# Kernel optimization log

Measured on AMD Instinct MI355X. Metric: run time of the kernel, lower is better.

The kernel has to match this reference:

```python
import jax, jax.numpy as jnp
import numpy as np

D_MODEL = 1024
NUM_HEADS = 16
NUM_KV_HEADS = 4
D_K = D_MODEL // NUM_HEADS  # 64
GROUP = NUM_HEADS // NUM_KV_HEADS  # 4
ROPE_BASE = 10000.0
NEG = -10000.0


def _rope_cos_sin(seq_len, d_k, dtype):
    # matches standard RotaryEmbedding: inv_freq over even dims, emb = cat(freqs, freqs)
    inv_freq = 1.0 / (ROPE_BASE ** (jnp.arange(0, d_k, 2, dtype=jnp.float32) / d_k))
    t = jnp.arange(seq_len, dtype=jnp.float32)
    freqs = jnp.einsum('s,f->sf', t, inv_freq)          # [S, d_k/2]
    emb = jnp.concatenate([freqs, freqs], axis=-1)       # [S, d_k]
    return jnp.cos(emb).astype(dtype), jnp.sin(emb).astype(dtype)


def _apply_rope(x, cos, sin):
    # x: [B, H, S, d_k]; cos/sin: [S, d_k] broadcast over B, H
    half = x.shape[-1] // 2
    x1, x2 = x[..., :half], x[..., half:]
    rotated = jnp.concatenate([-x2, x1], axis=-1)
    return x * cos + rotated * sin


def setup_inputs() -> dict:
    key = jax.random.key(0)
    ks = jax.random.split(key, 7)
    B, S = 2, 2048
    scale = 1.0 / np.sqrt(D_MODEL)
    return {
        'query': jax.random.normal(ks[0], (B, S, D_MODEL), dtype=jnp.float32),
        'key': jax.random.normal(ks[1], (B, S, D_MODEL), dtype=jnp.float32),
        'value': jax.random.normal(ks[2], (B, S, D_MODEL), dtype=jnp.float32),
        'Wq': jax.random.normal(ks[3], (D_MODEL, D_MODEL), dtype=jnp.float32) * scale,
        'Wk': jax.random.normal(ks[4], (NUM_KV_HEADS * D_K, D_MODEL), dtype=jnp.float32) * scale,
        'Wv': jax.random.normal(ks[5], (NUM_KV_HEADS * D_K, D_MODEL), dtype=jnp.float32) * scale,
        'Wo': jax.random.normal(ks[6], (D_MODEL, D_MODEL), dtype=jnp.float32) * scale,
    }


def reference(query, key, value, Wq, Wk, Wv, Wo):
    B, Sq, _ = query.shape
    Sk = key.shape[1]
    # projections (nn.Linear: x @ W.T)
    Q = (query @ Wq.T).reshape(B, Sq, NUM_HEADS, D_K).transpose(0, 2, 1, 3)      # [B,H,Sq,dk]
    K = (key @ Wk.T).reshape(B, Sk, NUM_KV_HEADS, D_K).transpose(0, 2, 1, 3)      # [B,Hkv,Sk,dk]
    V = (value @ Wv.T).reshape(B, Sk, NUM_KV_HEADS, D_K).transpose(0, 2, 1, 3)    # [B,Hkv,Sk,dk]
    # RoPE
    cos, sin = _rope_cos_sin(Sq, D_K, Q.dtype)
    Q = _apply_rope(Q, cos, sin)
    K = _apply_rope(K, cos[:Sk], sin[:Sk])
    # GQA attention without explicitly materializing expanded K/V:
    # group query heads as [B, Hkv, G, Sq, dk]
    Qg = Q.reshape(B, NUM_KV_HEADS, GROUP, Sq, D_K)
    scores = jnp.einsum('bhgqd,bhkd->bhgqk', Qg, K) / jnp.sqrt(jnp.float32(D_K))  # [B,Hkv,G,Sq,Sk]
    causal = jnp.tril(jnp.ones((Sq, Sk), dtype=bool))
    scores = jnp.where(causal, scores, jnp.float32(NEG))
    probs = jax.nn.softmax(scores, axis=-1)
    out = jnp.einsum('bhgqk,bhkd->bhgqd', probs, V)                                # [B,Hkv,G,Sq,dk]
    out = out.reshape(B, NUM_HEADS, Sq, D_K).transpose(0, 2, 1, 3).reshape(B, Sq, D_MODEL)
    return out @ Wo.T
```

## Files before the change

### kernel.cpp

```cpp
#include <hip/hip_runtime.h>
#include <hip/hip_bf16.h>
#include <stdint.h>

typedef __attribute__((ext_vector_type(4))) float f32x4;
typedef __attribute__((ext_vector_type(8))) short short8;

#define S_LEN 2048
#define BATCH 2
#define NH 16
#define NKV 4
#define DK 64
#define LOG2E 1.44269504f

__device__ __forceinline__ ushort f2bf(float f) {
  union { float f; uint32_t u; } v; v.f = f;
  uint32_t u = v.u;
  u += 0x7fff + ((u >> 16) & 1);
  return (ushort)(u >> 16);
}
__device__ __forceinline__ float bf2f(ushort h) {
  union { uint32_t u; float f; } v; v.u = ((uint32_t)h) << 16;
  return v.f;
}

__device__ __forceinline__ void gld16(const ushort* g, ushort* l) {
  __builtin_amdgcn_global_load_lds((const __attribute__((address_space(1))) void*)g,
                                   (__attribute__((address_space(3))) void*)l,
                                   16, 0, 0);
}

template<int CTRL>
__device__ __forceinline__ float dpp_movf(float x) {
  return __int_as_float(__builtin_amdgcn_update_dpp(0, __float_as_int(x), CTRL, 0xF, 0xF, true));
}
__device__ __forceinline__ float rowred_sum16(float v) {
  v += dpp_movf<0xB1>(v);
  v += dpp_movf<0x4E>(v);
  v += dpp_movf<0x141>(v);
  v += dpp_movf<0x140>(v);
  return v;
}

__global__ void cvt3_kernel(const float* __restrict__ q, const float* __restrict__ k,
                            const float* __restrict__ v, ushort* __restrict__ oq,
                            ushort* __restrict__ ok, ushort* __restrict__ ov) {
  int i = blockIdx.x * blockDim.x + threadIdx.x;
  if (i >= 1048576) return;
  const float* in = blockIdx.y == 0 ? q : (blockIdx.y == 1 ? k : v);
  ushort* out = blockIdx.y == 0 ? oq : (blockIdx.y == 1 ? ok : ov);
  float4 x = ((const float4*)in)[i];
  ushort4 o;
  o.x = f2bf(x.x); o.y = f2bf(x.y); o.z = f2bf(x.z); o.w = f2bf(x.w);
  ((ushort4*)out)[i] = o;
}

__global__ void cvtW_kernel(const float* __restrict__ w0, const float* __restrict__ w1,
                            const float* __restrict__ w2, const float* __restrict__ w3,
                            ushort* __restrict__ o0, ushort* __restrict__ o1,
                            ushort* __restrict__ o2, ushort* __restrict__ o3) {
  int y = blockIdx.y;
  int n4 = (y == 0 || y == 3) ? 262144 : 65536;
  int i = blockIdx.x * blockDim.x + threadIdx.x;
  if (i >= n4) return;
  const float* in = y == 0 ? w0 : y == 1 ? w1 : y == 2 ? w2 : w3;
  ushort* out = y == 0 ? o0 : y == 1 ? o1 : y == 2 ? o2 : o3;
  float4 x = ((const float4*)in)[i];
  ushort4 o;
  o.x = f2bf(x.x); o.y = f2bf(x.y); o.z = f2bf(x.z); o.w = f2bf(x.w);
  ((ushort4*)out)[i] = o;
}

__global__ void rope_table_kernel(float* __restrict__ tab) {
  int i = blockIdx.x * blockDim.x + threadIdx.x;
  int s = i >> 5, f = i & 31;
  float freq = (float)s * powf(10000.0f, -(float)f / 32.0f);
  tab[i] = cosf(freq);
  tab[65536 + i] = sinf(freq);
}

template<int EPI>
__device__ __forceinline__ void gemm_body(const ushort* __restrict__ A,
                                          const ushort* __restrict__ W,
                                          void* __restrict__ Cout,
                                          const float* __restrict__ tab,
                                          int N, int K, int bx, int by,
                                          ushort* Al, ushort* Wl) {
  const int t = threadIdx.x;
  const int lane = t & 63;
  const int w = t >> 6;
  const int wr = w >> 1, wc = w & 1;
  const int m0 = bx * 128, n0 = by * 128;
  const int g = lane >> 4, q16 = lane & 15;

  f32x4 acc[4][4] = {};

  const int lrow = lane >> 2, lcol = (lane & 3) * 8;
  const ushort* Ap = A + (size_t)(m0 + w * 32 + lrow) * K + lcol;
  const ushort* Wp = W + (size_t)(n0 + w * 32 + lrow) * K + lcol;
  ushort* Ab0 = &Al[(w * 32) * 32];
  ushort* Ab1 = &Al[(w * 32 + 16) * 32];
  ushort* Wb0 = &Wl[(w * 32) * 32];
  ushort* Wb1 = &Wl[(w * 32 + 16) * 32];

  const int KSTEPS = K >> 5;
  for (int kt = 0; kt < KSTEPS; ++kt) {
    const int k0 = kt << 5;
    __syncthreads();
    gld16(Ap + k0, Ab0);
    gld16(Ap + (size_t)16 * K + k0, Ab1);
    gld16(Wp + k0, Wb0);
    gld16(Wp + (size_t)16 * K + k0, Wb1);
    __syncthreads();
    short8 af[4], wf[4];
    #pragma unroll
    for (int i = 0; i < 4; ++i)
      af[i] = *(const short8*)&Al[(wr * 64 + i * 16 + q16) * 32 + g * 8];
    #pragma unroll
    for (int j = 0; j < 4; ++j)
      wf[j] = *(const short8*)&Wl[(wc * 64 + j * 16 + q16) * 32 + g * 8];
    #pragma unroll
    for (int i = 0; i < 4; ++i)
      #pragma unroll
      for (int j = 0; j < 4; ++j)
        acc[i][j] = __builtin_amdgcn_mfma_f32_16x16x32_bf16(af[i], wf[j], acc[i][j], 0, 0, 0);
  }

  if (EPI == 0) {
    #pragma unroll
    for (int i = 0; i < 4; ++i)
      #pragma unroll
      for (int j = 0; j < 4; ++j) {
        int row0 = m0 + wr * 64 + i * 16 + g * 4;
        int col  = n0 + wc * 64 + j * 16 + q16;
        #pragma unroll
        for (int r = 0; r < 4; ++r)
          ((float*)Cout)[(size_t)(row0 + r) * N + col] = acc[i][j][r];
      }
  } else if (EPI == 1 || EPI == 2) {
    const int NHE = (EPI == 1) ? NH : NKV;
    const float qscale = (EPI == 1) ? 0.125f * LOG2E : 1.0f;
    const int h = (n0 + wc * 64) >> 6;
    ushort* O = (ushort*)Cout;
    #pragma unroll
    for (int i = 0; i < 4; ++i)
      #pragma unroll
      for (int j = 0; j < 2; ++j) {
        const int d = j * 16 + q16;
        #pragma unroll
        for (int r = 0; r < 4; ++r) {
          int row = m0 + wr * 64 + i * 16 + g * 4 + r;
          int b = row >> 11, s = row & 2047;
          float x1 = acc[i][j][r], x2 = acc[i][j + 2][r];
          float c = tab[s * 32 + d], sn = tab[65536 + s * 32 + d];
          ushort* base = O + ((size_t)(b * NHE + h) * 2048 + s) * 64;
          base[d]      = f2bf((x1 * c - x2 * sn) * qscale);
          base[d + 32] = f2bf((x2 * c + x1 * sn) * qscale);
        }
      }
  } else {
    const int h = (n0 + wc * 64) >> 6;
    ushort* O = (ushort*)Cout;
    #pragma unroll
    for (int i = 0; i < 4; ++i) {
      int row0 = m0 + wr * 64 + i * 16 + g * 4;
      int b = row0 >> 11, s0 = row0 & 2047;
      #pragma unroll
      for (int j = 0; j < 4; ++j) {
        const int d = j * 16 + q16;
        ushort4 o;
        o.x = f2bf(acc[i][j][0]); o.y = f2bf(acc[i][j][1]);
        o.z = f2bf(acc[i][j][2]); o.w = f2bf(acc[i][j][3]);
        *(ushort4*)(O + ((size_t)(b * NKV + h) * 64 + d) * 2048 + s0) = o;
      }
    }
  }
}

__global__ __launch_bounds__(256) void qkv_gemm_kernel(
    const ushort* __restrict__ qbf, const ushort* __restrict__ wqb, ushort* __restrict__ Qh,
    const ushort* __restrict__ kbf, const ushort* __restrict__ wkb, ushort* __restrict__ Kh,
    const ushort* __restrict__ vbf, const ushort* __restrict__ wvb, ushort* __restrict__ Vt,
    const float* __restrict__ tab) {
  __shared__ ushort Al[128 * 32];
  __shared__ ushort Wl[128 * 32];
  const int id = blockIdx.x;
  if (id < 64) {
    gemm_body<2>(kbf, wkb, Kh, tab, 256, 1024, id & 31, id >> 5, Al, Wl);
  } else if (id < 128) {
    const int i = id - 64;
    gemm_body<3>(vbf, wvb, Vt, tab, 256, 1024, i & 31, i >> 5, Al, Wl);
  } else {
    const int i = id - 128;
    gemm_body<1>(qbf, wqb, Qh, tab, 1024, 1024, i & 31, i >> 5, Al, Wl);
  }
}

__global__ __launch_bounds__(256) void o_gemm_kernel(const ushort* __restrict__ AO,
                                                     const ushort* __restrict__ wob,
                                                     float* __restrict__ out) {
  __shared__ ushort Al[128 * 32];
  __shared__ ushort Wl[128 * 32];
  gemm_body<0>(AO, wob, out, nullptr, 1024, 1024, blockIdx.x & 31, blockIdx.x >> 5, Al, Wl);
}

__global__ __launch_bounds__(256) void fattn_kernel(const ushort* __restrict__ Qh,
                                                    const ushort* __restrict__ Kh,
                                                    const ushort* __restrict__ Vt,
                                                    ushort* __restrict__ AO) {
  __shared__ ushort Klds[2][4096];
  __shared__ ushort Vlds[2][4096];
  __shared__ ushort Plds[4][1024];
  const int t = threadIdx.x, lane = t & 63, wv = t >> 6;
  const int g = lane >> 4, q16 = lane & 15;

  const int hh = blockIdx.y;
  const int b = hh >> 4, h = hh & 15;
  const int kvh = h >> 2;
  const ushort* Kbase = Kh + (size_t)(b * 4 + kvh) * 2048 * 64;
  const ushort* Vbase = Vt + (size_t)(b * 4 + kvh) * 64 * 2048;

  const int r3 = lane >> 3, c3 = lane & 7;
  const int swz = (c3 ^ r3) << 3;
  const int call0 = wv * 2;

  for (int pass = 0; pass < 2; ++pass) {
    const int qt = pass ? (31 - (int)blockIdx.x) : (int)blockIdx.x;
    const int q0 = qt * 64 + wv * 16;
    const ushort* Qbase = Qh + ((size_t)hh * 2048 + q0) * 64;

    short8 aq[2];
    aq[0] = *(const short8*)(Qbase + (size_t)q16 * 64 + g * 8);
    aq[1] = *(const short8*)(Qbase + (size_t)q16 * 64 + 32 + g * 8);

    f32x4 acc[4] = {};
    float lsum[4] = {0.f, 0.f, 0.f, 0.f};

    const int nkb = qt + 1;

    __syncthreads();
    #pragma unroll
    for (int c = 0; c < 2; ++c) {
      int call = call0 + c;
      int row = call * 8 + r3;
      gld16(Kbase + (size_t)row * 64 + swz, &Klds[0][call * 512]);
      gld16(Vbase + (size_t)row * 2048 + swz, &Vlds[0][call * 512]);
    }

    int buf = 0;
    for (int kb = 0; kb < nkb; ++kb) {
      __syncthreads();
      if (kb + 1 < nkb) {
        const int k0n = (kb + 1) * 64;
        #pragma unroll
        for (int c = 0; c < 2; ++c) {
          int call = call0 + c;
          int row = call * 8 + r3;
          gld16(Kbase + (size_t)(k0n + row) * 64 + swz, &Klds[buf ^ 1][call * 512]);
          gld16(Vbase + (size_t)row * 2048 + k0n + swz, &Vlds[buf ^ 1][call * 512]);
        }
      }
      const ushort* Kl = Klds[buf];
      const ushort* Vl = Vlds[buf];
      const int k0 = kb * 64;

      f32x4 sA[4] = {};
      __builtin_amdgcn_s_setprio(1);
      #pragma unroll
      for (int kk = 0; kk < 2; ++kk)
        #pragma unroll
        for (int nt = 0; nt < 4; ++nt) {
          int row = nt * 16 + q16;
          int slot = ((kk << 2) | g) ^ (q16 & 7);
          short8 bk = *(const short8*)(Kl + row * 64 + (slot << 3));
          sA[nt] = __builtin_amdgcn_mfma_f32_16x16x32_bf16(aq[kk], bk, sA[nt], 0, 0, 0);
        }
      __builtin_amdgcn_s_setprio(0);

      if (kb == nkb - 1) {
        #pragma unroll
        for (int nt = 0; nt < 4; ++nt)
          #pragma unroll
          for (int r = 0; r < 4; ++r) {
            int col = k0 + nt * 16 + q16, row = q0 + g * 4 + r;
            if (col > row) sA[nt][r] = -1e30f;
          }
      }

      float ps[4][4];
      #pragma unroll
      for (int nt = 0; nt < 4; ++nt)
        #pragma unroll
        for (int r = 0; r < 4; ++r)
          ps[nt][r] = exp2f(sA[nt][r]);
      #pragma unroll
      for (int r = 0; r < 4; ++r)
        lsum[r] += (ps[0][r] + ps[1][r]) + (ps[2][r] + ps[3][r]);

      #pragma unroll
      for (int nt = 0; nt < 4; ++nt)
        #pragma unroll
        for (int r = 0; r < 4; ++r) {
          int pr = g * 4 + r;
          Plds[wv][pr * 64 + ((nt * 16 + q16) ^ ((pr & 7) << 3))] = f2bf(ps[nt][r]);
        }
      __builtin_amdgcn_s_setprio(1);
      #pragma unroll
      for (int kk2 = 0; kk2 < 2; ++kk2) {
        int slot = ((kk2 << 2) | g) ^ (q16 & 7);
        short8 pa = *(const short8*)(&Plds[wv][q16 * 64 + (slot << 3)]);
        #pragma unroll
        for (int dt = 0; dt < 4; ++dt) {
          int rv = dt * 16 + q16;
          short8 bv = *(const short8*)(Vl + rv * 64 + (slot << 3));
          acc[dt] = __builtin_amdgcn_mfma_f32_16x16x32_bf16(pa, bv, acc[dt], 0, 0, 0);
        }
      }
      __builtin_amdgcn_s_setprio(0);

      buf ^= 1;
    }

    float linv[4];
    #pragma unroll
    for (int r = 0; r < 4; ++r) linv[r] = 1.0f / rowred_sum16(lsum[r]);
    #pragma unroll
    for (int dt = 0; dt < 4; ++dt)
      #pragma unroll
      for (int r = 0; r < 4; ++r) {
        float o = acc[dt][r] * linv[r];
        AO[((size_t)(b * 2048) + q0 + g * 4 + r) * 1024 + h * 64 + dt * 16 + q16] = f2bf(o);
      }
  }
}

extern "C" void kernel_launch(void* const* d_in, const int* in_sizes, int n_in,
                              void* d_out, int out_size, void* d_ws, size_t ws_size,
                              hipStream_t stream) {
  const float* query = (const float*)d_in[0];
  const float* key   = (const float*)d_in[1];
  const float* value = (const float*)d_in[2];
  const float* Wq    = (const float*)d_in[3];
  const float* Wk    = (const float*)d_in[4];
  const float* Wv    = (const float*)d_in[5];
  const float* Wo    = (const float*)d_in[6];
  float* out = (float*)d_out;

  char* ws = (char*)d_ws;
  size_t off = 0;
  auto alloc = [&](size_t bytes) {
    void* p = ws + off; off += (bytes + 255) & ~255ULL; return p;
  };
  ushort* qbf = (ushort*)alloc(4096ULL * 1024 * 2);
  ushort* kbf = (ushort*)alloc(4096ULL * 1024 * 2);
  ushort* vbf = (ushort*)alloc(4096ULL * 1024 * 2);
  ushort* wqb = (ushort*)alloc(1024ULL * 1024 * 2);
  ushort* wkb = (ushort*)alloc(256ULL * 1024 * 2);
  ushort* wvb = (ushort*)alloc(256ULL * 1024 * 2);
  ushort* wob = (ushort*)alloc(1024ULL * 1024 * 2);
  ushort* Qh  = (ushort*)alloc(4096ULL * 1024 * 2);
  ushort* Kh  = (ushort*)alloc(4096ULL * 256 * 2);
  ushort* Vt  = (ushort*)alloc(4096ULL * 256 * 2);
  ushort* AO  = (ushort*)alloc(4096ULL * 1024 * 2);
  float*  tab = (float*)alloc(2048ULL * 32 * 4 * 2);

  cvt3_kernel<<<dim3(4096, 3), 256, 0, stream>>>(query, key, value, qbf, kbf, vbf);
  cvtW_kernel<<<dim3(1024, 4), 256, 0, stream>>>(Wq, Wk, Wv, Wo, wqb, wkb, wvb, wob);
  rope_table_kernel<<<256, 256, 0, stream>>>((float*)tab);

  qkv_gemm_kernel<<<384, 256, 0, stream>>>(qbf, wqb, Qh, kbf, wkb, Kh, vbf, wvb, Vt, (float*)tab);

  fattn_kernel<<<dim3(16, 32), 256, 0, stream>>>(Qh, Kh, Vt, AO);

  o_gemm_kernel<<<256, 256, 0, stream>>>(AO, wob, out);
}
```

Before: 121.6 us.

## Fuse preprocessing kernels, halve GEMM M-tile, use native exp and bf16 convert

Merges the three conversion and RoPE-table kernels into one launch to cut launch overhead. Shrinks the GEMM M-tile from 128 to 64 rows so the QKV and output projections launch twice as many blocks, improving CU fill on a large GPU at the cost of less operand reuse per block. Switches the softmax exponent from exp2f with a log2e-folded scale to __expf, and uses the library bf16 conversion.

```diff
diff --git a/kernel.cpp b/kernel.cpp
--- a/kernel.cpp
+++ b/kernel.cpp
@@ -10,13 +10,10 @@
 #define NH 16
 #define NKV 4
 #define DK 64
-#define LOG2E 1.44269504f
 
 __device__ __forceinline__ ushort f2bf(float f) {
-  union { float f; uint32_t u; } v; v.f = f;
-  uint32_t u = v.u;
-  u += 0x7fff + ((u >> 16) & 1);
-  return (ushort)(u >> 16);
+  __hip_bfloat16 h = __float2bfloat16(f);
+  ushort u; __builtin_memcpy(&u, &h, 2); return u;
 }
 __device__ __forceinline__ float bf2f(ushort h) {
   union { uint32_t u; float f; } v; v.u = ((uint32_t)h) << 16;
@@ -41,41 +38,43 @@
   return v;
 }
 
-__global__ void cvt3_kernel(const float* __restrict__ q, const float* __restrict__ k,
-                            const float* __restrict__ v, ushort* __restrict__ oq,
-                            ushort* __restrict__ ok, ushort* __restrict__ ov) {
-  int i = blockIdx.x * blockDim.x + threadIdx.x;
-  if (i >= 1048576) return;
-  const float* in = blockIdx.y == 0 ? q : (blockIdx.y == 1 ? k : v);
-  ushort* out = blockIdx.y == 0 ? oq : (blockIdx.y == 1 ? ok : ov);
-  float4 x = ((const float4*)in)[i];
-  ushort4 o;
-  o.x = f2bf(x.x); o.y = f2bf(x.y); o.z = f2bf(x.z); o.w = f2bf(x.w);
-  ((ushort4*)out)[i] = o;
-}
-
-__global__ void cvtW_kernel(const float* __restrict__ w0, const float* __restrict__ w1,
-                            const float* __restrict__ w2, const float* __restrict__ w3,
-                            ushort* __restrict__ o0, ushort* __restrict__ o1,
-                            ushort* __restrict__ o2, ushort* __restrict__ o3) {
-  int y = blockIdx.y;
-  int n4 = (y == 0 || y == 3) ? 262144 : 65536;
-  int i = blockIdx.x * blockDim.x + threadIdx.x;
-  if (i >= n4) return;
-  const float* in = y == 0 ? w0 : y == 1 ? w1 : y == 2 ? w2 : w3;
-  ushort* out = y == 0 ? o0 : y == 1 ? o1 : y == 2 ? o2 : o3;
-  float4 x = ((const float4*)in)[i];
-  ushort4 o;
-  o.x = f2bf(x.x); o.y = f2bf(x.y); o.z = f2bf(x.z); o.w = f2bf(x.w);
-  ((ushort4*)out)[i] = o;
-}
-
-__global__ void rope_table_kernel(float* __restrict__ tab) {
-  int i = blockIdx.x * blockDim.x + threadIdx.x;
-  int s = i >> 5, f = i & 31;
-  float freq = (float)s * powf(10000.0f, -(float)f / 32.0f);
-  tab[i] = cosf(freq);
-  tab[65536 + i] = sinf(freq);
+__global__ void preproc_kernel(const float* __restrict__ q, const float* __restrict__ k,
+                               const float* __restrict__ v, ushort* __restrict__ oq,
+                               ushort* __restrict__ ok, ushort* __restrict__ ov,
+                               const float* __restrict__ w0, const float* __restrict__ w1,
+                               const float* __restrict__ w2, const float* __restrict__ w3,
+                               ushort* __restrict__ o0, ushort* __restrict__ o1,
+                               ushort* __restrict__ o2, ushort* __restrict__ o3,
+                               float* __restrict__ tab) {
+  const int id = blockIdx.x, tid = threadIdx.x;
+  if (id < 12288) {
+    int y = id >> 12;
+    int i = ((id & 4095) << 8) + tid;
+    const float* in = y == 0 ? q : (y == 1 ? k : v);
+    ushort* out = y == 0 ? oq : (y == 1 ? ok : ov);
+    float4 x = ((const float4*)in)[i];
+    ushort4 o;
+    o.x = f2bf(x.x); o.y = f2bf(x.y); o.z = f2bf(x.z); o.w = f2bf(x.w);
+    ((ushort4*)out)[i] = o;
+  } else if (id < 16384) {
+    int wid = id - 12288;
+    int y = wid >> 10;
+    int n4 = (y == 0 || y == 3) ? 262144 : 65536;
+    int i = ((wid & 1023) << 8) + tid;
+    if (i >= n4) return;
+    const float* in = y == 0 ? w0 : y == 1 ? w1 : y == 2 ? w2 : w3;
+    ushort* out = y == 0 ? o0 : y == 1 ? o1 : y == 2 ? o2 : o3;
+    float4 x = ((const float4*)in)[i];
+    ushort4 o;
+    o.x = f2bf(x.x); o.y = f2bf(x.y); o.z = f2bf(x.z); o.w = f2bf(x.w);
+    ((ushort4*)out)[i] = o;
+  } else {
+    int j = ((id - 16384) << 8) + tid;
+    int s = j >> 5, f = j & 31;
+    float freq = (float)s * powf(10000.0f, -(float)f / 32.0f);
+    tab[j] = cosf(freq);
+    tab[65536 + j] = sinf(freq);
+  }
 }
 
 template<int EPI>
@@ -89,16 +88,16 @@
   const int lane = t & 63;
   const int w = t >> 6;
   const int wr = w >> 1, wc = w & 1;
-  const int m0 = bx * 128, n0 = by * 128;
+  const int m0 = bx * 64, n0 = by * 128;
   const int g = lane >> 4, q16 = lane & 15;
 
-  f32x4 acc[4][4] = {};
+  f32x4 acc[2][4] = {};
 
   const int lrow = lane >> 2, lcol = (lane & 3) * 8;
-  const ushort* Ap = A + (size_t)(m0 + w * 32 + lrow) * K + lcol;
-  const ushort* Wp = W + (size_t)(n0 + w * 32 + lrow) * K + lcol;
-  ushort* Ab0 = &Al[(w * 32) * 32];
-  ushort* Ab1 = &Al[(w * 32 + 16) * 32];
+  const ushort* Ap  = A + (size_t)(m0 + w * 16 + lrow) * K + lcol;
+  const ushort* Wp0 = W + (size_t)(n0 + w * 32 + lrow) * K + lcol;
+  const ushort* Wp1 = W + (size_t)(n0 + w * 32 + 16 + lrow) * K + lcol;
+  ushort* Ab  = &Al[(w * 16) * 32];
   ushort* Wb0 = &Wl[(w * 32) * 32];
   ushort* Wb1 = &Wl[(w * 32 + 16) * 32];
 
@@ -106,20 +105,19 @@
   for (int kt = 0; kt < KSTEPS; ++kt) {
     const int k0 = kt << 5;
     __syncthreads();
-    gld16(Ap + k0, Ab0);
-    gld16(Ap + (size_t)16 * K + k0, Ab1);
-    gld16(Wp + k0, Wb0);
-    gld16(Wp + (size_t)16 * K + k0, Wb1);
+    gld16(Ap + k0, Ab);
+    gld16(Wp0 + k0, Wb0);
+    gld16(Wp1 + k0, Wb1);
     __syncthreads();
-    short8 af[4], wf[4];
-    #pragma unroll
-    for (int i = 0; i < 4; ++i)
-      af[i] = *(const short8*)&Al[(wr * 64 + i * 16 + q16) * 32 + g * 8];
+    short8 af[2], wf[4];
+    #pragma unroll
+    for (int i = 0; i < 2; ++i)
+      af[i] = *(const short8*)&Al[(wr * 32 + i * 16 + q16) * 32 + g * 8];
     #pragma unroll
     for (int j = 0; j < 4; ++j)
       wf[j] = *(const short8*)&Wl[(wc * 64 + j * 16 + q16) * 32 + g * 8];
     #pragma unroll
-    for (int i = 0; i < 4; ++i)
+    for (int i = 0; i < 2; ++i)
       #pragma unroll
       for (int j = 0; j < 4; ++j)
         acc[i][j] = __builtin_amdgcn_mfma_f32_16x16x32_bf16(af[i], wf[j], acc[i][j], 0, 0, 0);
@@ -127,10 +125,10 @@
 
   if (EPI == 0) {
     #pragma unroll
-    for (int i = 0; i < 4; ++i)
+    for (int i = 0; i < 2; ++i)
       #pragma unroll
       for (int j = 0; j < 4; ++j) {
-        int row0 = m0 + wr * 64 + i * 16 + g * 4;
+        int row0 = m0 + wr * 32 + i * 16 + g * 4;
         int col  = n0 + wc * 64 + j * 16 + q16;
         #pragma unroll
         for (int r = 0; r < 4; ++r)
@@ -138,17 +136,17 @@
       }
   } else if (EPI == 1 || EPI == 2) {
     const int NHE = (EPI == 1) ? NH : NKV;
-    const float qscale = (EPI == 1) ? 0.125f * LOG2E : 1.0f;
+    const float qscale = (EPI == 1) ? 0.125f : 1.0f;
     const int h = (n0 + wc * 64) >> 6;
     ushort* O = (ushort*)Cout;
     #pragma unroll
-    for (int i = 0; i < 4; ++i)
+    for (int i = 0; i < 2; ++i)
       #pragma unroll
       for (int j = 0; j < 2; ++j) {
         const int d = j * 16 + q16;
         #pragma unroll
         for (int r = 0; r < 4; ++r) {
-          int row = m0 + wr * 64 + i * 16 + g * 4 + r;
+          int row = m0 + wr * 32 + i * 16 + g * 4 + r;
           int b = row >> 11, s = row & 2047;
           float x1 = acc[i][j][r], x2 = acc[i][j + 2][r];
           float c = tab[s * 32 + d], sn = tab[65536 + s * 32 + d];
@@ -161,8 +159,8 @@
     const int h = (n0 + wc * 64) >> 6;
     ushort* O = (ushort*)Cout;
     #pragma unroll
-    for (int i = 0; i < 4; ++i) {
-      int row0 = m0 + wr * 64 + i * 16 + g * 4;
+    for (int i = 0; i < 2; ++i) {
+      int row0 = m0 + wr * 32 + i * 16 + g * 4;
       int b = row0 >> 11, s0 = row0 & 2047;
       #pragma unroll
       for (int j = 0; j < 4; ++j) {
@@ -181,26 +179,26 @@
     const ushort* __restrict__ kbf, const ushort* __restrict__ wkb, ushort* __restrict__ Kh,
     const ushort* __restrict__ vbf, const ushort* __restrict__ wvb, ushort* __restrict__ Vt,
     const float* __restrict__ tab) {
-  __shared__ ushort Al[128 * 32];
+  __shared__ ushort Al[64 * 32];
   __shared__ ushort Wl[128 * 32];
   const int id = blockIdx.x;
-  if (id < 64) {
-    gemm_body<2>(kbf, wkb, Kh, tab, 256, 1024, id & 31, id >> 5, Al, Wl);
-  } else if (id < 128) {
-    const int i = id - 64;
-    gemm_body<3>(vbf, wvb, Vt, tab, 256, 1024, i & 31, i >> 5, Al, Wl);
+  if (id < 128) {
+    gemm_body<2>(kbf, wkb, Kh, tab, 256, 1024, id & 63, id >> 6, Al, Wl);
+  } else if (id < 256) {
+    const int i = id - 128;
+    gemm_body<3>(vbf, wvb, Vt, tab, 256, 1024, i & 63, i >> 6, Al, Wl);
   } else {
-    const int i = id - 128;
-    gemm_body<1>(qbf, wqb, Qh, tab, 1024, 1024, i & 31, i >> 5, Al, Wl);
+    const int i = id - 256;
+    gemm_body<1>(qbf, wqb, Qh, tab, 1024, 1024, i & 63, i >> 6, Al, Wl);
   }
 }
 
 __global__ __launch_bounds__(256) void o_gemm_kernel(const ushort* __restrict__ AO,
                                                      const ushort* __restrict__ wob,
                                                      float* __restrict__ out) {
-  __shared__ ushort Al[128 * 32];
+  __shared__ ushort Al[64 * 32];
   __shared__ ushort Wl[128 * 32];
-  gemm_body<0>(AO, wob, out, nullptr, 1024, 1024, blockIdx.x & 31, blockIdx.x >> 5, Al, Wl);
+  gemm_body<0>(AO, wob, out, nullptr, 1024, 1024, blockIdx.x & 63, blockIdx.x >> 6, Al, Wl);
 }
 
 __global__ __launch_bounds__(256) void fattn_kernel(const ushort* __restrict__ Qh,
@@ -291,7 +289,7 @@
       for (int nt = 0; nt < 4; ++nt)
         #pragma unroll
         for (int r = 0; r < 4; ++r)
-          ps[nt][r] = exp2f(sA[nt][r]);
+          ps[nt][r] = __expf(sA[nt][r]);
       #pragma unroll
       for (int r = 0; r < 4; ++r)
         lsum[r] += (ps[0][r] + ps[1][r]) + (ps[2][r] + ps[3][r]);
@@ -363,13 +361,13 @@
   ushort* AO  = (ushort*)alloc(4096ULL * 1024 * 2);
   float*  tab = (float*)alloc(2048ULL * 32 * 4 * 2);
 
-  cvt3_kernel<<<dim3(4096, 3), 256, 0, stream>>>(query, key, value, qbf, kbf, vbf);
-  cvtW_kernel<<<dim3(1024, 4), 256, 0, stream>>>(Wq, Wk, Wv, Wo, wqb, wkb, wvb, wob);
-  rope_table_kernel<<<256, 256, 0, stream>>>((float*)tab);
-
-  qkv_gemm_kernel<<<384, 256, 0, stream>>>(qbf, wqb, Qh, kbf, wkb, Kh, vbf, wvb, Vt, (float*)tab);
+  preproc_kernel<<<16640, 256, 0, stream>>>(query, key, value, qbf, kbf, vbf,
+                                            Wq, Wk, Wv, Wo, wqb, wkb, wvb, wob,
+                                            (float*)tab);
+
+  qkv_gemm_kernel<<<768, 256, 0, stream>>>(qbf, wqb, Qh, kbf, wkb, Kh, vbf, wvb, Vt, (float*)tab);
 
   fattn_kernel<<<dim3(16, 32), 256, 0, stream>>>(Qh, Kh, Vt, AO);
 
-  o_gemm_kernel<<<256, 256, 0, stream>>>(AO, wob, out);
-}
+  o_gemm_kernel<<<512, 256, 0, stream>>>(AO, wob, out);
+}
```

After: 105.0 us. -13.7%, faster.
